# Optimization experiments

Hardware: AMD Instinct MI355X
Metric: run time of the kernel (lower is better)

## Reference

```python
import jax, jax.numpy as jnp
import numpy as np

B, T_CHAR, E, N_CHARS, T_TAG = 128, 256, 512, 128, 32


def _rn(k, shape, scale=1.0):
    return jax.random.normal(k, shape, dtype=jnp.float32) * scale


def setup_inputs() -> dict:
    key = jax.random.key(0)
    ks = jax.random.split(key, 24)
    W = 0.05  # param init scale
    tgt_idx = jax.random.randint(ks[4], (B, T_CHAR), 0, N_CHARS)
    return {
        "char_encoding": _rn(ks[0], (B, T_CHAR, E)),
        "char_hn": _rn(ks[1], (2, B, E // 2)),
        "char_cn": _rn(ks[2], (2, B, E // 2)),
        "tag_encoding": _rn(ks[3], (B, T_TAG, E)),
        "true_output_seq": jax.nn.one_hot(tgt_idx, N_CHARS, dtype=jnp.float32),
        # LSTMCell(n_chars -> E), torch gate order i,f,g,o
        "lstm_Wih": _rn(ks[5], (4 * E, N_CHARS), W),
        "lstm_Whh": _rn(ks[6], (4 * E, E), W),
        "lstm_bih": jnp.zeros((4 * E,), jnp.float32),
        "lstm_bhh": jnp.zeros((4 * E,), jnp.float32),
        # char MultiheadAttention (1 head)
        "ca_Wq": _rn(ks[7], (E, E), W), "ca_Wk": _rn(ks[8], (E, E), W), "ca_Wv": _rn(ks[9], (E, E), W),
        "ca_bq": jnp.zeros((E,), jnp.float32), "ca_bk": jnp.zeros((E,), jnp.float32), "ca_bv": jnp.zeros((E,), jnp.float32),
        "ca_Wo": _rn(ks[10], (E, E), W), "ca_bo": jnp.zeros((E,), jnp.float32),
        # tag MultiheadAttention (1 head)
        "ta_Wq": _rn(ks[11], (E, E), W), "ta_Wk": _rn(ks[12], (E, E), W), "ta_Wv": _rn(ks[13], (E, E), W),
        "ta_bq": jnp.zeros((E,), jnp.float32), "ta_bk": jnp.zeros((E,), jnp.float32), "ta_bv": jnp.zeros((E,), jnp.float32),
        "ta_Wo": _rn(ks[14], (E, E), W), "ta_bo": jnp.zeros((E,), jnp.float32),
        # output Linear(2E -> n_chars)
        "out_W": _rn(ks[15], (N_CHARS, 2 * E), W),
        "out_b": jnp.zeros((N_CHARS,), jnp.float32),
    }


def _attend(h, enc_K, enc_V, Wq, bq, Wo, bo):
    # single-head torch MHA: scale query by 1/sqrt(embed_dim)
    q = (h @ Wq.T + bq) * (1.0 / np.sqrt(E))          # [B,E]
    scores = jnp.einsum('be,bse->bs', q, enc_K)        # [B,S]
    a = jax.nn.softmax(scores, axis=-1)
    ctx = jnp.einsum('bs,bse->be', a, enc_V)           # [B,E]
    return ctx @ Wo.T + bo


def reference(char_encoding, char_hn, char_cn, tag_encoding, true_output_seq,
              lstm_Wih, lstm_Whh, lstm_bih, lstm_bhh,
              ca_Wq, ca_Wk, ca_Wv, ca_bq, ca_bk, ca_bv, ca_Wo, ca_bo,
              ta_Wq, ta_Wk, ta_Wv, ta_bq, ta_bk, ta_bv, ta_Wo, ta_bo,
              out_W, out_b):
    # K/V projections are step-invariant: hoist out of the decode loop
    Kc = char_encoding @ ca_Wk.T + ca_bk               # [B,Tc,E]
    Vc = char_encoding @ ca_Wv.T + ca_bv
    Kt = tag_encoding @ ta_Wk.T + ta_bk                # [B,Tt,E]
    Vt = tag_encoding @ ta_Wv.T + ta_bv

    h0 = jnp.concatenate([char_hn[0], char_hn[1]], axis=-1)  # [B,E]
    c0 = jnp.concatenate([char_cn[0], char_cn[1]], axis=-1)

    # teacher forcing: step 0 input is zeros, step t uses true_output_seq[:, t, :]
    x0 = jnp.zeros((char_encoding.shape[0], true_output_seq.shape[-1]), char_encoding.dtype)
    xs = jnp.concatenate([x0[:, None, :], true_output_seq[:, 1:, :]], axis=1)
    xs = jnp.swapaxes(xs, 0, 1)                        # [T,B,n_chars]

    def step(carry, x_t):
        h, c = carry
        gates = x_t @ lstm_Wih.T + lstm_bih + h @ lstm_Whh.T + lstm_bhh
        i, f, g, o = jnp.split(gates, 4, axis=-1)
        c1 = jax.nn.sigmoid(f) * c + jax.nn.sigmoid(i) * jnp.tanh(g)
        h1 = jax.nn.sigmoid(o) * jnp.tanh(c1)
        char_ctx = _attend(h1, Kc, Vc, ca_Wq, ca_bq, ca_Wo, ca_bo)
        tag_ctx = _attend(h1, Kt, Vt, ta_Wq, ta_bq, ta_Wo, ta_bo)
        agg = jax.nn.relu(jnp.concatenate([char_ctx, tag_ctx], axis=-1))  # [B,2E]
        out = agg @ out_W.T + out_b                    # [B,n_chars]
        return (h1, c1), out

    _, outs = jax.lax.scan(step, (h0, c0), xs)         # outs: [T,B,n_chars]
    return jnp.swapaxes(outs, 0, 1)                    # [B,T,n_chars]
```

## Files before the change

### kernel.cpp

```cpp
#include <hip/hip_runtime.h>
#include <cstdint>

#define BB 128
#define TT 256
#define EE 512
#define NC 128
#define STAG 32

#define NWG 64
#define SB 4
#define SC 16
#define NKV 2304

using bf = unsigned short;
typedef __attribute__((ext_vector_type(8))) short short8;
typedef __attribute__((ext_vector_type(8))) unsigned short ushort8;
typedef __attribute__((ext_vector_type(16))) float f32x16;
typedef unsigned long long u64;

static __device__ __forceinline__ float bf_lo(uint32_t u) { return __uint_as_float(u << 16); }
static __device__ __forceinline__ float bf_hi(uint32_t u) { return __uint_as_float(u & 0xFFFF0000u); }
static __device__ __forceinline__ float bfu(bf x) { return __uint_as_float(((uint32_t)x) << 16); }
static __device__ __forceinline__ uint32_t f2bf(float f) {
    uint32_t u = __float_as_uint(f);
    return (u + 0x7FFFu + ((u >> 16) & 1u)) >> 16;
}
static __device__ __forceinline__ float sigmoidf_(float x) { return 1.f / (1.f + expf(-x)); }

static __device__ __forceinline__ void bf8exp(const uint4 u, float* f) {
    f[0] = bf_lo(u.x); f[1] = bf_hi(u.x); f[2] = bf_lo(u.y); f[3] = bf_hi(u.y);
    f[4] = bf_lo(u.z); f[5] = bf_hi(u.z); f[6] = bf_lo(u.w); f[7] = bf_hi(u.w);
}

static __device__ __forceinline__ uint4 pack8bf(float4 a, float4 b) {
    uint4 o;
    o.x = (f2bf(a.y) << 16) | f2bf(a.x);
    o.y = (f2bf(a.w) << 16) | f2bf(a.z);
    o.z = (f2bf(b.y) << 16) | f2bf(b.x);
    o.w = (f2bf(b.w) << 16) | f2bf(b.z);
    return o;
}

static __device__ __forceinline__ uint32_t relu2bf(uint32_t x) {
    uint32_t lo = x & 0xFFFFu, hi = x >> 16;
    lo = (lo & 0x8000u) ? 0u : lo;
    hi = (hi & 0x8000u) ? 0u : hi;
    return lo | (hi << 16);
}

__global__ void diag_ws(float* __restrict__ out, float v, int n) {
    int i = blockIdx.x * 256 + threadIdx.x;
    if (i < n) out[i] = v;
}

__global__ void conv_f2b(const float* __restrict__ s, bf* __restrict__ d, int n) {
    int i = (blockIdx.x * 256 + threadIdx.x) * 4;
    if (i >= n) return;
    float4 v = *(const float4*)(s + i);
    ushort4 o = { (bf)f2bf(v.x), (bf)f2bf(v.y), (bf)f2bf(v.z), (bf)f2bf(v.w) };
    *(ushort4*)(d + i) = o;
}

struct W8 { const float* p[8]; };
__global__ void conv_w8(W8 ws, bf* __restrict__ d) {
    int m = blockIdx.y;
    int i = (blockIdx.x * 256 + threadIdx.x) * 4;
    float4 v = *(const float4*)(ws.p[m] + i);
    ushort4 o = { (bf)f2bf(v.x), (bf)f2bf(v.y), (bf)f2bf(v.z), (bf)f2bf(v.w) };
    *(ushort4*)(d + (size_t)m * 262144 + i) = o;
}

__global__ void h0_pack(const float* __restrict__ hn, bf* __restrict__ Hext) {
    int id = blockIdx.x * 256 + threadIdx.x;
    int b = id >> 9, e = id & 511;
    float v = (e < 256) ? hn[(size_t)b * 256 + e] : hn[(size_t)(BB + b) * 256 + (e - 256)];
    Hext[((size_t)(e >> 3) * BB + b) * 8 + (e & 7)] = (bf)f2bf(v);
}

__global__ void bt_prep2(const float* __restrict__ Whh, bf* __restrict__ Btg2) {
    int id = blockIdx.x * 256 + threadIdx.x;
    int row = id >> 6, chunk = (id & 63) * 8;
    int cg = row >> 7, n = row & 127;
    int r = (n & 3) * 512 + cg * 32 + (n >> 2);
    const float* src = Whh + (size_t)r * 512 + chunk;
    ushort8 o;
#pragma unroll
    for (int i = 0; i < 8; ++i) o[i] = (bf)f2bf(src[i]);
    *(ushort8*)(Btg2 + (size_t)row * 512 + chunk) = o;
}

__global__ void x_prep(const float* __restrict__ tos, int* __restrict__ xidx,
                       float* __restrict__ xval) {
    int id = blockIdx.x * 256 + threadIdx.x;
    int t = id >> 7, b = id & 127;
    int idx = 0; float val = 0.f;
    if (t > 0) {
        const float* row = tos + ((size_t)b * TT + t) * NC;
        for (int k = 0; k < NC; ++k) {
            float v = row[k];
            if (v != 0.f) { idx = k; val = v; }
        }
    }
    xidx[(size_t)t * BB + b] = idx;
    xval[(size_t)t * BB + b] = val;
}

static __device__ __forceinline__ int lds_off(int row, int colbyte) {
    return row * 128 + (colbyte ^ ((row & 7) << 4));
}

static __device__ __forceinline__ void worker_gemm(
    const float* __restrict__ Af, const bf* __restrict__ Wb,
    const float* __restrict__ bias, bf* __restrict__ C,
    int bm, int bn, char* smem)
{
    bf* As = (bf*)smem;
    bf* Bs = (bf*)(smem + 16384);
    const int tid = threadIdx.x;
    const int w = tid >> 6, l = tid & 63;
    const int wr = (w >> 1) * 64, wc = (w & 1) * 64;

    f32x16 acc[2][2];
#pragma unroll
    for (int i = 0; i < 2; ++i)
#pragma unroll
        for (int j = 0; j < 2; ++j)
#pragma unroll
            for (int r = 0; r < 16; ++r) acc[i][j][r] = 0.f;

    const int srow = tid >> 3;
    const int scolb = (tid & 7) * 16;
    const int scole = (tid & 7) * 8;

    for (int k0 = 0; k0 < 512; k0 += 64) {
#pragma unroll
        for (int pass = 0; pass < 4; ++pass) {
            int row = pass * 32 + srow;
            const float* ap = Af + (size_t)(bm + row) * 512 + k0 + scole;
            float4 v0 = *(const float4*)ap;
            float4 v1 = *(const float4*)(ap + 4);
            *(uint4*)(smem + lds_off(row, scolb)) = pack8bf(v0, v1);
            uint4 vb = *(const uint4*)(Wb + (size_t)(bn + row) * 512 + k0 + scole);
            *(uint4*)((char*)Bs + lds_off(row, scolb)) = vb;
        }
        __syncthreads();
#pragma unroll
        for (int kt = 0; kt < 4; ++kt) {
            const int cb = kt * 32 + (l >> 5) * 16;
            short8 af[2], bfr[2];
#pragma unroll
            for (int i = 0; i < 2; ++i) {
                af[i]  = *(const short8*)((char*)As + lds_off(wr + i * 32 + (l & 31), cb));
                bfr[i] = *(const short8*)((char*)Bs + lds_off(wc + i * 32 + (l & 31), cb));
            }
#pragma unroll
            for (int i = 0; i < 2; ++i)
#pragma unroll
                for (int j = 0; j < 2; ++j)
                    acc[i][j] = __builtin_amdgcn_mfma_f32_32x32x16_bf16(af[i], bfr[j], acc[i][j], 0, 0, 0);
        }
        __syncthreads();
    }

#pragma unroll
    for (int i = 0; i < 2; ++i)
#pragma unroll
        for (int j = 0; j < 2; ++j) {
            int n = bn + wc + j * 32 + (l & 31);
            float bv = bias[n];
#pragma unroll
            for (int r = 0; r < 16; ++r) {
                int m = bm + wr + i * 32 + (r & 3) + 8 * (r >> 2) + 4 * (l >> 5);
                C[(size_t)m * 512 + n] = (bf)f2bf(acc[i][j][r] + bv);
            }
        }
}

struct KVArgs {
    const float *Ac, *At;
    const bf *WcK, *WcV, *WtK, *WtV;
    const float *bcK, *bcV, *btK, *btV;
    bf *Kc, *Vc, *Kt, *Vt;
};

__global__ __launch_bounds__(256, 1) void lstm_fused(
    bf* __restrict__ Hext,
    const bf* __restrict__ Btg2,
    const float* __restrict__ Wih,
    const float* __restrict__ bih, const float* __restrict__ bhh,
    const float* __restrict__ cn,
    const int* __restrict__ xidx, const float* __restrict__ xval,
    char* __restrict__ flags,
    KVArgs kv)
{
    __shared__ __align__(16) char smem[66048];

    const int gb = blockIdx.x, tid = threadIdx.x;

    if (gb >= NWG) {
        int w = gb - NWG;
        if (w < 2048) {
            int v = w >> 10, t = w & 1023;
            worker_gemm(kv.Ac, v ? kv.WcV : kv.WcK, v ? kv.bcV : kv.bcK,
                        v ? kv.Vc : kv.Kc, (t >> 2) * 128, (t & 3) * 128, smem);
        } else {
            int w2 = w - 2048;
            int v = w2 >> 7, t = w2 & 127;
            worker_gemm(kv.At, v ? kv.WtV : kv.WtK, v ? kv.btV : kv.btK,
                        v ? kv.Vt : kv.Kt, (t >> 2) * 128, (t & 3) * 128, smem);
        }
        return;
    }

    bf*    Alds   = (bf*)smem;
    float* gatesf = (float*)smem;
    bf*    wihtp  = (bf*)(smem + 32768);
    float* biass  = (float*)(smem + 65536);

    const int g = gb;
    const int bh = g >> 4, cg = g & 15;

    for (int x = tid; x < 128 * NC; x += 256) {
        int n = x >> 7, k = x & 127;
        int r = (n & 3) * 512 + cg * 32 + (n >> 2);
        wihtp[k * 128 + n] = (bf)f2bf(Wih[(size_t)r * NC + k]);
    }
    if (tid < 128) {
        int r = (tid & 3) * 512 + cg * 32 + (tid >> 2);
        biass[tid] = bih[r] + bhh[r];
    }

    const int b_loc = tid >> 3, u = tid & 7;
    const int b_glob = bh * 32 + b_loc;
    float creg[4];
    {
        int j0 = cg * 32 + u * 4;
        const float* csrc = (cg < 8) ? (cn + (size_t)b_glob * 256 + j0)
                                     : (cn + (size_t)(BB + b_glob) * 256 + (j0 - 256));
#pragma unroll
        for (int i = 0; i < 4; ++i) creg[i] = csrc[i];
    }

    const int wv = tid >> 6, l = tid & 63;

    short8 breg[32];
    {
        const bf* bsrc = Btg2 + ((size_t)(cg * 128 + wv * 32 + (l & 31)) * 512)
                       + (l >> 5) * 8;
#pragma unroll
        for (int kt = 0; kt < 32; ++kt) breg[kt] = *(const short8*)(bsrc + kt * 16);
    }
    __syncthreads();

    const int sb = tid & 31, sg0 = tid >> 5;
    const int dst_lane = sb | ((sg0 & 1) << 5);
    bf* dstbase = Alds + (size_t)(sg0 >> 1) * 512 + dst_lane * 8;

    u64* Hw = (u64*)Hext;
    const size_t SLABB = (size_t)BB * EE * 2;
    const size_t SLAB64 = (size_t)BB * EE / 4;
    const size_t hst_off = (size_t)(cg * 4 + (u >> 1)) * 256 + b_glob * 2 + (u & 1);
    const bf* ards = Alds + l * 8;

    for (int t = 0; t < TT; ++t) {
        const char* At = (const char*)Hext + (size_t)t * SLABB
                       + (size_t)sg0 * 2048 + (size_t)(bh * 32 + sb) * 16;
        uint4 areg[8];
#pragma unroll
        for (int i = 0; i < 8; ++i) {
            asm volatile("global_load_dwordx4 %0, %1, off sc0 sc1"
                         : "=v"(areg[i]) : "v"(At + (size_t)i * 16384));
        }
        float xv = xval[(size_t)t * BB + b_glob];
        int   xi = xidx[(size_t)t * BB + b_glob];
        asm volatile("s_waitcnt vmcnt(0)" ::: "memory");
        __builtin_amdgcn_sched_barrier(0);
#pragma unroll
        for (int i = 0; i < 8; ++i)
            *(uint4*)(dstbase + (size_t)i * 2048) = areg[i];
        __syncthreads();

        f32x16 acc0, acc1;
#pragma unroll
        for (int i = 0; i < 16; ++i) { acc0[i] = 0.f; acc1[i] = 0.f; }
#pragma unroll
        for (int kt = 0; kt < 32; kt += 2) {
            short8 a0 = *(const short8*)(ards + (size_t)kt * 512);
            short8 a1 = *(const short8*)(ards + (size_t)(kt + 1) * 512);
            acc0 = __builtin_amdgcn_mfma_f32_32x32x16_bf16(a0, breg[kt], acc0, 0, 0, 0);
            acc1 = __builtin_amdgcn_mfma_f32_32x32x16_bf16(a1, breg[kt + 1], acc1, 0, 0, 0);
        }
        __syncthreads();
#pragma unroll
        for (int r = 0; r < 16; ++r) {
            int m = (r & 3) + 8 * (r >> 2) + 4 * (l >> 5);
            gatesf[m * 132 + wv * 32 + (l & 31)] = acc0[r] + acc1[r];
        }
        __syncthreads();

        {
            union { ushort4 v; u64 uu; } hout;
#pragma unroll
            for (int i = 0; i < 4; ++i) {
                int nb = (u * 4 + i) * 4;
                float4 ga  = *(const float4*)&gatesf[b_loc * 132 + nb];
                float4 bb4 = *(const float4*)&biass[nb];
                ushort4 xw = *(const ushort4*)&wihtp[xi * 128 + nb];
                float a0 = ga.x + bb4.x + xv * bfu(xw.x);
                float a1 = ga.y + bb4.y + xv * bfu(xw.y);
                float a2 = ga.z + bb4.z + xv * bfu(xw.z);
                float a3 = ga.w + bb4.w + xv * bfu(xw.w);
                float ig = sigmoidf_(a0);
                float fg = sigmoidf_(a1);
                float gg = tanhf(a2);
                float og = sigmoidf_(a3);
                creg[i] = fg * creg[i] + ig * gg;
                float hnew = og * tanhf(creg[i]);
                hout.v[i] = (bf)f2bf(hnew);
            }
            __hip_atomic_store(Hw + (size_t)(t + 1) * SLAB64 + hst_off, hout.uu,
                               __ATOMIC_RELAXED, __HIP_MEMORY_SCOPE_AGENT);
        }

        if (t + 1 < TT) {
            asm volatile("s_waitcnt vmcnt(0)" ::: "memory");
            __syncthreads();
            char* fb = flags + (size_t)(t + 1) * (SB * 2048) + (size_t)bh * 2048;
            if (tid == 0)
                __hip_atomic_store((int*)(fb + (size_t)cg * 128), 1,
                                   __ATOMIC_RELAXED, __HIP_MEMORY_SCOPE_SYSTEM);
            if (tid < 64) {
                const int* fp = (const int*)(fb + (size_t)(tid & 15) * 128);
                while (true) {
                    int v = __hip_atomic_load(fp, __ATOMIC_RELAXED,
                                              __HIP_MEMORY_SCOPE_SYSTEM);
                    if (__all(v != 0)) break;
                    __builtin_amdgcn_s_sleep(1);
                }
            }
            asm volatile("" ::: "memory");
            __syncthreads();
        }
    }
}

template <bool AH2>
__global__ __launch_bounds__(256) void gemm_mfma(
    const bf* __restrict__ A, const bf* __restrict__ Wb,
    const float* __restrict__ bias, bf* __restrict__ C,
    int M, float alpha)
{
    __shared__ __align__(16) bf As[128 * 64];
    __shared__ __align__(16) bf Bs[128 * 64];
    const int tid = threadIdx.x;
    const int bm = blockIdx.y * 128, bn = blockIdx.x * 128;
    const int w = tid >> 6, l = tid & 63;
    const int wr = (w >> 1) * 64, wc = (w & 1) * 64;

    f32x16 acc[2][2];
#pragma unroll
    for (int i = 0; i < 2; ++i)
#pragma unroll
        for (int j = 0; j < 2; ++j)
#pragma unroll
            for (int r = 0; r < 16; ++r) acc[i][j][r] = 0.f;

    const int srow = tid >> 3;
    const int scolb = (tid & 7) * 16;
    const int scole = (tid & 7) * 8;

    for (int k0 = 0; k0 < 512; k0 += 64) {
#pragma unroll
        for (int pass = 0; pass < 4; ++pass) {
            int row = pass * 32 + srow;
            const bf* ap;
            if constexpr (AH2) {
                int m = bm + row; int tt = m >> 7, bb_ = m & 127;
                int grp = (k0 + scole) >> 3;
                ap = A + ((((size_t)tt * 64 + grp) * BB + bb_) << 3);
            } else {
                ap = A + (size_t)(bm + row) * 512 + k0 + scole;
            }
            uint4 va = *(const uint4*)ap;
            *(uint4*)((char*)As + lds_off(row, scolb)) = va;
            uint4 vb = *(const uint4*)(Wb + (size_t)(bn + row) * 512 + k0 + scole);
            *(uint4*)((char*)Bs + lds_off(row, scolb)) = vb;
        }
        __syncthreads();
#pragma unroll
        for (int kt = 0; kt < 4; ++kt) {
            const int cb = kt * 32 + (l >> 5) * 16;
            short8 af[2], bfr[2];
#pragma unroll
            for (int i = 0; i < 2; ++i) {
                af[i]  = *(const short8*)((char*)As + lds_off(wr + i * 32 + (l & 31), cb));
                bfr[i] = *(const short8*)((char*)Bs + lds_off(wc + i * 32 + (l & 31), cb));
            }
#pragma unroll
            for (int i = 0; i < 2; ++i)
#pragma unroll
                for (int j = 0; j < 2; ++j)
                    acc[i][j] = __builtin_amdgcn_mfma_f32_32x32x16_bf16(af[i], bfr[j], acc[i][j], 0, 0, 0);
        }
        __syncthreads();
    }

#pragma unroll
    for (int i = 0; i < 2; ++i)
#pragma unroll
        for (int j = 0; j < 2; ++j) {
            int n = bn + wc + j * 32 + (l & 31);
            float bv = bias ? bias[n] : 0.f;
#pragma unroll
            for (int r = 0; r < 16; ++r) {
                int m = bm + wr + i * 32 + (r & 3) + 8 * (r >> 2) + 4 * (l >> 5);
                C[(size_t)m * 512 + n] = (bf)f2bf((acc[i][j][r] + bv) * alpha);
            }
        }
}

__global__ __launch_bounds__(256) void gemm_out(
    const bf* __restrict__ A1, const bf* __restrict__ A2,
    const bf* __restrict__ Wo,
    const float* __restrict__ bias, float* __restrict__ out)
{
    __shared__ __align__(16) bf As[128 * 64];
    __shared__ __align__(16) bf Bs[128 * 64];
    const int tid = threadIdx.x;
    const int bm = blockIdx.x * 128;
    const int w = tid >> 6, l = tid & 63;
    const int wr = (w >> 1) * 64, wc = (w & 1) * 64;

    f32x16 acc[2][2];
#pragma unroll
    for (int i = 0; i < 2; ++i)
#pragma unroll
        for (int j = 0; j < 2; ++j)
#pragma unroll
            for (int r = 0; r < 16; ++r) acc[i][j][r] = 0.f;

    const int srow = tid >> 3;
    const int scolb = (tid & 7) * 16;
    const int scole = (tid & 7) * 8;

    for (int k0 = 0; k0 < 1024; k0 += 64) {
        const bf* Asrc = (k0 < 512) ? A1 : A2;
        const int kk = k0 & 511;
#pragma unroll
        for (int pass = 0; pass < 4; ++pass) {
            int row = pass * 32 + srow;
            uint4 va = *(const uint4*)(Asrc + (size_t)(bm + row) * 512 + kk + scole);
            va.x = relu2bf(va.x); va.y = relu2bf(va.y);
            va.z = relu2bf(va.z); va.w = relu2bf(va.w);
            *(uint4*)((char*)As + lds_off(row, scolb)) = va;
            uint4 vb = *(const uint4*)(Wo + (size_t)row * 1024 + k0 + scole);
            *(uint4*)((char*)Bs + lds_off(row, scolb)) = vb;
        }
        __syncthreads();
#pragma unroll
        for (int kt = 0; kt < 4; ++kt) {
            const int cb = kt * 32 + (l >> 5) * 16;
            short8 af[2], bfr[2];
#pragma unroll
            for (int i = 0; i < 2; ++i) {
                af[i]  = *(const short8*)((char*)As + lds_off(wr + i * 32 + (l & 31), cb));
                bfr[i] = *(const short8*)((char*)Bs + lds_off(wc + i * 32 + (l & 31), cb));
            }
#pragma unroll
            for (int i = 0; i < 2; ++i)
#pragma unroll
                for (int j = 0; j < 2; ++j)
                    acc[i][j] = __builtin_amdgcn_mfma_f32_32x32x16_bf16(af[i], bfr[j], acc[i][j], 0, 0, 0);
        }
        __syncthreads();
    }

#pragma unroll
    for (int i = 0; i < 2; ++i)
#pragma unroll
        for (int j = 0; j < 2; ++j) {
            int n = wc + j * 32 + (l & 31);
            float bv = bias[n];
#pragma unroll
            for (int r = 0; r < 16; ++r) {
                int m = bm + wr + i * 32 + (r & 3) + 8 * (r >> 2) + 4 * (l >> 5);
                int tt = m >> 7, bb_ = m & 127;
                out[((size_t)bb_ * TT + tt) * NC + n] = acc[i][j][r] + bv;
            }
        }
}

template <int S>
__global__ __launch_bounds__(256) void attn_kernel(
    const bf* __restrict__ Q, const bf* __restrict__ Km,
    const bf* __restrict__ Vm, bf* __restrict__ ctx)
{
    constexpr int RT = 16;
    int t0 = blockIdx.x * RT;
    int b = blockIdx.y;
    int tid = threadIdx.x;

    __shared__ __align__(16) float qs[RT][EE];
    __shared__ float ps[RT][S];
    __shared__ float red[RT][17];
    __shared__ float rowsum[RT];

#pragma unroll
    for (int i = 0; i < RT * EE / (256 * 8); ++i) {
        int x = (i * 256 + tid) * 8;
        int r = x / EE, e = x % EE;
        uint4 u = *(const uint4*)&Q[((size_t)(t0 + r) * BB + b) * EE + e];
        float f[8]; bf8exp(u, f);
#pragma unroll
        for (int q = 0; q < 8; ++q) qs[r][e + q] = f[q];
    }
    __syncthreads();

    if constexpr (S >= 256) {
        int s = tid;
        float acc[RT] = {};
        const uint4* kp = (const uint4*)&Km[((size_t)b * S + s) * EE];
        for (int e8 = 0; e8 < EE / 8; ++e8) {
            float kf[8]; bf8exp(kp[e8], kf);
#pragma unroll
            for (int r = 0; r < RT; ++r) {
                float a = 0.f;
#pragma unroll
                for (int q = 0; q < 8; ++q) a += qs[r][e8 * 8 + q] * kf[q];
                acc[r] += a;
            }
        }
#pragma unroll
        for (int r = 0; r < RT; ++r) ps[r][s] = acc[r];
    } else {
        constexpr int KS = 256 / S;
        constexpr int EC = EE / KS;
        __shared__ float pp[KS][RT][S];
        int s = tid & (S - 1);
        int kq = tid / S;
        float acc[RT] = {};
        const uint4* kp = (const uint4*)&Km[((size_t)b * S + s) * EE + kq * EC];
        for (int e8 = 0; e8 < EC / 8; ++e8) {
            float kf[8]; bf8exp(kp[e8], kf);
#pragma unroll
            for (int r = 0; r < RT; ++r) {
                float a = 0.f;
#pragma unroll
                for (int q = 0; q < 8; ++q) a += qs[r][kq * EC + e8 * 8 + q] * kf[q];
                acc[r] += a;
            }
        }
#pragma unroll
        for (int r = 0; r < RT; ++r) pp[kq][r][s] = acc[r];
        __syncthreads();
        for (int x = tid; x < RT * S; x += 256) {
            int r = x / S, ss = x % S;
            float v = 0.f;
#pragma unroll
            for (int q = 0; q < KS; ++q) v += pp[q][r][ss];
            ps[r][ss] = v;
        }
    }
    __syncthreads();

    {
        int r = tid >> 4, l = tid & 15;
        float m = -1e30f;
        for (int s = l; s < S; s += 16) m = fmaxf(m, ps[r][s]);
        red[r][l] = m;
        __syncthreads();
        for (int w = 8; w >= 1; w >>= 1) {
            if (l < w) red[r][l] = fmaxf(red[r][l], red[r][l + w]);
            __syncthreads();
        }
        float mm = red[r][0];
        float sum = 0.f;
        for (int s = l; s < S; s += 16) {
            float e = expf(ps[r][s] - mm);
            ps[r][s] = e;
            sum += e;
        }
        __syncthreads();
        red[r][l] = sum;
        __syncthreads();
        for (int w = 8; w >= 1; w >>= 1) {
            if (l < w) red[r][l] += red[r][l + w];
            __syncthreads();
        }
        if (l == 0) rowsum[r] = red[r][0];
    }
    __syncthreads();

    {
        float acc0[RT] = {}, acc1[RT] = {};
        for (int s = 0; s < S; ++s) {
            float v0 = bfu(Vm[((size_t)b * S + s) * EE + tid]);
            float v1 = bfu(Vm[((size_t)b * S + s) * EE + tid + 256]);
#pragma unroll
            for (int r = 0; r < RT; ++r) {
                float p = ps[r][s];
                acc0[r] += p * v0;
                acc1[r] += p * v1;
            }
        }
#pragma unroll
        for (int r = 0; r < RT; ++r) {
            float inv = 1.f / rowsum[r];
            size_t row = (size_t)(t0 + r) * BB + b;
            ctx[row * EE + tid] = (bf)f2bf(acc0[r] * inv);
            ctx[row * EE + tid + 256] = (bf)f2bf(acc1[r] * inv);
        }
    }
}

extern "C" void kernel_launch(void* const* d_in, const int* in_sizes, int n_in,
                              void* d_out, int out_size, void* d_ws, size_t ws_size,
                              hipStream_t stream) {
    const float* char_enc = (const float*)d_in[0];
    const float* char_hn  = (const float*)d_in[1];
    const float* char_cn  = (const float*)d_in[2];
    const float* tag_enc  = (const float*)d_in[3];
    const float* tos      = (const float*)d_in[4];
    const float* Wih = (const float*)d_in[5];
    const float* Whh = (const float*)d_in[6];
    const float* bih = (const float*)d_in[7];
    const float* bhh = (const float*)d_in[8];
    const float* caWq = (const float*)d_in[9],  *caWk = (const float*)d_in[10], *caWv = (const float*)d_in[11];
    const float* cabq = (const float*)d_in[12], *cabk = (const float*)d_in[13], *cabv = (const float*)d_in[14];
    const float* caWo = (const float*)d_in[15], *cabo = (const float*)d_in[16];
    const float* taWq = (const float*)d_in[17], *taWk = (const float*)d_in[18], *taWv = (const float*)d_in[19];
    const float* tabq = (const float*)d_in[20], *tabk = (const float*)d_in[21], *tabv = (const float*)d_in[22];
    const float* taWo = (const float*)d_in[23], *tabo = (const float*)d_in[24];
    const float* outW = (const float*)d_in[25], *outb = (const float*)d_in[26];
    float* out = (float*)d_out;

    const size_t SZ  = (size_t)TT * BB * EE;
    const size_t SZT = (size_t)BB * STAG * EE;
    const size_t SLAB = (size_t)BB * EE;
    const size_t HEXT = SZ + SLAB;
    const size_t FLAGB = (size_t)TT * SB * 2048;

    const size_t NEED = FLAGB + HEXT * 2 + 4 * SZ * 2 + 2 * SZT * 2
                      + (size_t)SC * 128 * EE * 2 + (size_t)TT * BB * 8
                      + (8 * 262144 + 131072) * 2;
    if (ws_size < NEED) {
        diag_ws<<<dim3((out_size + 255) / 256), dim3(256), 0, stream>>>(
            out, (float)((double)ws_size / 1048576.0), out_size);
        return;
    }

    char* w = (char*)d_ws;
    char* flags = w;             w += FLAGB;
    bf* Hext = (bf*)w;           w += HEXT * 2;
    bf* Kc = (bf*)w;             w += SZ * 2;
    bf* Vc = (bf*)w;             w += SZ * 2;
    bf* Qc = (bf*)w;             w += SZ * 2;
    bf* Qt = (bf*)w;             w += SZ * 2;
    bf* Kt = (bf*)w;             w += SZT * 2;
    bf* Vt = (bf*)w;             w += SZT * 2;
    bf* Btg2 = (bf*)w;           w += (size_t)SC * 128 * EE * 2;
    int* xidx = (int*)w;         w += (size_t)TT * BB * 4;
    float* xval = (float*)w;     w += (size_t)TT * BB * 4;
    bf* Wbf = (bf*)w;            w += 8 * 262144 * 2;
    bf* WoutB = (bf*)w;          w += 131072 * 2;

    const bf* Hh = Hext + SLAB;
    const float QSCALE = 0.044194173824159216f;
    const int M = TT * BB;

    bf* WbcaK = Wbf + 0 * 262144; bf* WbcaV = Wbf + 1 * 262144;
    bf* WbcaQ = Wbf + 2 * 262144; bf* WbcaO = Wbf + 3 * 262144;
    bf* WbtaK = Wbf + 4 * 262144; bf* WbtaV = Wbf + 5 * 262144;
    bf* WbtaQ = Wbf + 6 * 262144; bf* WbtaO = Wbf + 7 * 262144;

    hipMemsetAsync(flags, 0, FLAGB, stream);
    h0_pack<<<dim3(256), dim3(256), 0, stream>>>(char_hn, Hext);
    bt_prep2<<<dim3(512), dim3(256), 0, stream>>>(Whh, Btg2);
    x_prep<<<dim3(128), dim3(256), 0, stream>>>(tos, xidx, xval);
    W8 w8; w8.p[0] = caWk; w8.p[1] = caWv; w8.p[2] = caWq; w8.p[3] = caWo;
    w8.p[4] = taWk; w8.p[5] = taWv; w8.p[6] = taWq; w8.p[7] = taWo;
    conv_w8<<<dim3(256, 8), dim3(256), 0, stream>>>(w8, Wbf);
    conv_f2b<<<dim3(128), dim3(256), 0, stream>>>(outW, WoutB, 131072);

    KVArgs kv;
    kv.Ac = char_enc; kv.At = tag_enc;
    kv.WcK = WbcaK; kv.WcV = WbcaV; kv.WtK = WbtaK; kv.WtV = WbtaV;
    kv.bcK = cabk; kv.bcV = cabv; kv.btK = tabk; kv.btV = tabv;
    kv.Kc = Kc; kv.Vc = Vc; kv.Kt = Kt; kv.Vt = Vt;
    lstm_fused<<<dim3(NWG + NKV), dim3(256), 0, stream>>>(
        Hext, Btg2, Wih, bih, bhh, char_cn, xidx, xval, flags, kv);

    gemm_mfma<true><<<dim3(4, 256), dim3(256), 0, stream>>>(Hh, WbcaQ, cabq, Qc, M, QSCALE);
    gemm_mfma<true><<<dim3(4, 256), dim3(256), 0, stream>>>(Hh, WbtaQ, tabq, Qt, M, QSCALE);

    attn_kernel<256><<<dim3(TT / 16, BB), dim3(256), 0, stream>>>(Qc, Kc, Vc, Qc);
    attn_kernel<32><<<dim3(TT / 16, BB), dim3(256), 0, stream>>>(Qt, Kt, Vt, Qt);

    gemm_mfma<false><<<dim3(4, 256), dim3(256), 0, stream>>>(Qc, WbcaO, cabo, Kc, M, 1.f);
    gemm_mfma<false><<<dim3(4, 256), dim3(256), 0, stream>>>(Qt, WbtaO, tabo, Vc, M, 1.f);

    gemm_out<<<dim3(256), dim3(256), 0, stream>>>(Kc, Vc, WoutB, outb, out);
}
```

Baseline: 1.716 ms.

## Fuse Q projection, attention, and output projection into one MFMA kernel per attention

Replaces the separate Q-projection GEMMs, scalar-FMA attention kernels and output-projection GEMMs with a single attn_fused kernel per attention that computes Q, the scores, the softmax, P·V and the Wo projection on MFMA, keeping intermediates in LDS. The K/V worker GEMMs now write V transposed (per batch, feature-major) so the P·V MFMA can read contiguous operands. This removes the global round trips for Q and the context plus the fp32 scalar attention math. In exchange, each block rereads Wq, Wo and K/V straight from global memory without LDS staging, and the grid is smaller (8x128 blocks at one block per CU), which may limit occupancy.

```diff
diff --git a/kernel.cpp b/kernel.cpp
--- a/kernel.cpp
+++ b/kernel.cpp
@@ -18,19 +18,12 @@
 typedef __attribute__((ext_vector_type(16))) float f32x16;
 typedef unsigned long long u64;
 
-static __device__ __forceinline__ float bf_lo(uint32_t u) { return __uint_as_float(u << 16); }
-static __device__ __forceinline__ float bf_hi(uint32_t u) { return __uint_as_float(u & 0xFFFF0000u); }
 static __device__ __forceinline__ float bfu(bf x) { return __uint_as_float(((uint32_t)x) << 16); }
 static __device__ __forceinline__ uint32_t f2bf(float f) {
     uint32_t u = __float_as_uint(f);
     return (u + 0x7FFFu + ((u >> 16) & 1u)) >> 16;
 }
 static __device__ __forceinline__ float sigmoidf_(float x) { return 1.f / (1.f + expf(-x)); }
-
-static __device__ __forceinline__ void bf8exp(const uint4 u, float* f) {
-    f[0] = bf_lo(u.x); f[1] = bf_hi(u.x); f[2] = bf_lo(u.y); f[3] = bf_hi(u.y);
-    f[4] = bf_lo(u.z); f[5] = bf_hi(u.z); f[6] = bf_lo(u.w); f[7] = bf_hi(u.w);
-}
 
 static __device__ __forceinline__ uint4 pack8bf(float4 a, float4 b) {
     uint4 o;
@@ -109,6 +102,7 @@
     return row * 128 + (colbyte ^ ((row & 7) << 4));
 }
 
+template <int MODE>
 static __device__ __forceinline__ void worker_gemm(
     const float* __restrict__ Af, const bf* __restrict__ Wb,
     const float* __restrict__ bias, bf* __restrict__ C,
@@ -139,7 +133,7 @@
             const float* ap = Af + (size_t)(bm + row) * 512 + k0 + scole;
             float4 v0 = *(const float4*)ap;
             float4 v1 = *(const float4*)(ap + 4);
-            *(uint4*)(smem + lds_off(row, scolb)) = pack8bf(v0, v1);
+            *(uint4*)((char*)As + lds_off(row, scolb)) = pack8bf(v0, v1);
             uint4 vb = *(const uint4*)(Wb + (size_t)(bn + row) * 512 + k0 + scole);
             *(uint4*)((char*)Bs + lds_off(row, scolb)) = vb;
         }
@@ -171,7 +165,16 @@
 #pragma unroll
             for (int r = 0; r < 16; ++r) {
                 int m = bm + wr + i * 32 + (r & 3) + 8 * (r >> 2) + 4 * (l >> 5);
-                C[(size_t)m * 512 + n] = (bf)f2bf(acc[i][j][r] + bv);
+                bf v = (bf)f2bf(acc[i][j][r] + bv);
+                if constexpr (MODE == 0) {
+                    C[(size_t)m * 512 + n] = v;
+                } else if constexpr (MODE == 1) {
+                    int b = m >> 8, s = m & 255;
+                    C[((size_t)b * 512 + n) * 256 + s] = v;
+                } else {
+                    int b = m >> 5, s = m & 31;
+                    C[((size_t)b * 512 + n) * 32 + s] = v;
+                }
             }
         }
 }
@@ -180,7 +183,7 @@
     const float *Ac, *At;
     const bf *WcK, *WcV, *WtK, *WtV;
     const float *bcK, *bcV, *btK, *btV;
-    bf *Kc, *Vc, *Kt, *Vt;
+    bf *Kc, *VcT, *Kt, *VtT;
 };
 
 __global__ __launch_bounds__(256, 1) void lstm_fused(
@@ -199,15 +202,17 @@
 
     if (gb >= NWG) {
         int w = gb - NWG;
-        if (w < 2048) {
-            int v = w >> 10, t = w & 1023;
-            worker_gemm(kv.Ac, v ? kv.WcV : kv.WcK, v ? kv.bcV : kv.bcK,
-                        v ? kv.Vc : kv.Kc, (t >> 2) * 128, (t & 3) * 128, smem);
+        if (w < 1024) {
+            worker_gemm<0>(kv.Ac, kv.WcK, kv.bcK, kv.Kc, (w >> 2) * 128, (w & 3) * 128, smem);
+        } else if (w < 2048) {
+            int t = w - 1024;
+            worker_gemm<1>(kv.Ac, kv.WcV, kv.bcV, kv.VcT, (t >> 2) * 128, (t & 3) * 128, smem);
+        } else if (w < 2176) {
+            int t = w - 2048;
+            worker_gemm<0>(kv.At, kv.WtK, kv.btK, kv.Kt, (t >> 2) * 128, (t & 3) * 128, smem);
         } else {
-            int w2 = w - 2048;
-            int v = w2 >> 7, t = w2 & 127;
-            worker_gemm(kv.At, v ? kv.WtV : kv.WtK, v ? kv.btV : kv.btK,
-                        v ? kv.Vt : kv.Kt, (t >> 2) * 128, (t & 3) * 128, smem);
+            int t = w - 2176;
+            worker_gemm<2>(kv.At, kv.WtV, kv.btV, kv.VtT, (t >> 2) * 128, (t & 3) * 128, smem);
         }
         return;
     }
@@ -344,79 +349,159 @@
     }
 }
 
-template <bool AH2>
-__global__ __launch_bounds__(256) void gemm_mfma(
-    const bf* __restrict__ A, const bf* __restrict__ Wb,
-    const float* __restrict__ bias, bf* __restrict__ C,
-    int M, float alpha)
+template <int S>
+__global__ __launch_bounds__(256, 1) void attn_fused(
+    const bf* __restrict__ Hext,
+    const bf* __restrict__ Wq, const float* __restrict__ bq,
+    const bf* __restrict__ Km,
+    const bf* __restrict__ VT,
+    const bf* __restrict__ Wo, const float* __restrict__ bo,
+    bf* __restrict__ occ)
 {
-    __shared__ __align__(16) bf As[128 * 64];
-    __shared__ __align__(16) bf Bs[128 * 64];
-    const int tid = threadIdx.x;
-    const int bm = blockIdx.y * 128, bn = blockIdx.x * 128;
-    const int w = tid >> 6, l = tid & 63;
-    const int wr = (w >> 1) * 64, wc = (w & 1) * 64;
-
-    f32x16 acc[2][2];
-#pragma unroll
-    for (int i = 0; i < 2; ++i)
-#pragma unroll
-        for (int j = 0; j < 2; ++j)
-#pragma unroll
-            for (int r = 0; r < 16; ++r) acc[i][j][r] = 0.f;
-
-    const int srow = tid >> 3;
-    const int scolb = (tid & 7) * 16;
-    const int scole = (tid & 7) * 8;
-
-    for (int k0 = 0; k0 < 512; k0 += 64) {
-#pragma unroll
-        for (int pass = 0; pass < 4; ++pass) {
-            int row = pass * 32 + srow;
-            const bf* ap;
-            if constexpr (AH2) {
-                int m = bm + row; int tt = m >> 7, bb_ = m & 127;
-                int grp = (k0 + scole) >> 3;
-                ap = A + ((((size_t)tt * 64 + grp) * BB + bb_) << 3);
-            } else {
-                ap = A + (size_t)(bm + row) * 512 + k0 + scole;
-            }
-            uint4 va = *(const uint4*)ap;
-            *(uint4*)((char*)As + lds_off(row, scolb)) = va;
-            uint4 vb = *(const uint4*)(Wb + (size_t)(bn + row) * 512 + k0 + scole);
-            *(uint4*)((char*)Bs + lds_off(row, scolb)) = vb;
-        }
-        __syncthreads();
-#pragma unroll
-        for (int kt = 0; kt < 4; ++kt) {
-            const int cb = kt * 32 + (l >> 5) * 16;
-            short8 af[2], bfr[2];
-#pragma unroll
-            for (int i = 0; i < 2; ++i) {
-                af[i]  = *(const short8*)((char*)As + lds_off(wr + i * 32 + (l & 31), cb));
-                bfr[i] = *(const short8*)((char*)Bs + lds_off(wc + i * 32 + (l & 31), cb));
-            }
-#pragma unroll
-            for (int i = 0; i < 2; ++i)
-#pragma unroll
-                for (int j = 0; j < 2; ++j)
-                    acc[i][j] = __builtin_amdgcn_mfma_f32_32x32x16_bf16(af[i], bfr[j], acc[i][j], 0, 0, 0);
-        }
-        __syncthreads();
-    }
-
-#pragma unroll
-    for (int i = 0; i < 2; ++i)
-#pragma unroll
-        for (int j = 0; j < 2; ++j) {
-            int n = bn + wc + j * 32 + (l & 31);
-            float bv = bias ? bias[n] : 0.f;
+    constexpr int SP = S + 8;
+    __shared__ __align__(16) bf    Qs[32][520];
+    __shared__ __align__(16) float scs[32][SP];
+    __shared__ __align__(16) bf    Ps[32][SP];
+
+    const float QSCALE = 0.044194173824159216f;
+    const int t0 = blockIdx.x * 32, b = blockIdx.y;
+    const int tid = threadIdx.x, wv = tid >> 6, l = tid & 63;
+    const int lm = l & 31, lh = l >> 5;
+
+    {
+        f32x16 qa[4];
+#pragma unroll
+        for (int nt = 0; nt < 4; ++nt)
+#pragma unroll
+            for (int r = 0; r < 16; ++r) qa[nt][r] = 0.f;
+#pragma unroll 4
+        for (int kt = 0; kt < 32; ++kt) {
+            short8 a = *(const short8*)(Hext
+                + (((size_t)(t0 + lm + 1) * 64 + kt * 2 + lh) * 1024 + (size_t)b * 8));
+#pragma unroll
+            for (int nt = 0; nt < 4; ++nt) {
+                int n = wv * 128 + nt * 32 + lm;
+                short8 w = *(const short8*)(Wq + (size_t)n * 512 + kt * 16 + lh * 8);
+                qa[nt] = __builtin_amdgcn_mfma_f32_32x32x16_bf16(a, w, qa[nt], 0, 0, 0);
+            }
+        }
+#pragma unroll
+        for (int nt = 0; nt < 4; ++nt) {
+            int n = wv * 128 + nt * 32 + lm;
+            float bv = bq[n];
 #pragma unroll
             for (int r = 0; r < 16; ++r) {
-                int m = bm + wr + i * 32 + (r & 3) + 8 * (r >> 2) + 4 * (l >> 5);
-                C[(size_t)m * 512 + n] = (bf)f2bf((acc[i][j][r] + bv) * alpha);
-            }
-        }
+                int m = (r & 3) + 8 * (r >> 2) + 4 * lh;
+                Qs[m][n] = (bf)f2bf((qa[nt][r] + bv) * QSCALE);
+            }
+        }
+    }
+    __syncthreads();
+
+    {
+        constexpr int NJ = (S == 256) ? 2 : 1;
+        f32x16 sa[NJ];
+#pragma unroll
+        for (int j = 0; j < NJ; ++j)
+#pragma unroll
+            for (int r = 0; r < 16; ++r) sa[j][r] = 0.f;
+#pragma unroll 4
+        for (int kt = 0; kt < 32; ++kt) {
+            short8 a = *(const short8*)&Qs[lm][kt * 16 + lh * 8];
+#pragma unroll
+            for (int j = 0; j < NJ; ++j) {
+                int s = ((S == 256) ? (wv * 64 + j * 32) : 0) + lm;
+                short8 k8 = *(const short8*)(Km + ((size_t)b * S + s) * 512 + kt * 16 + lh * 8);
+                sa[j] = __builtin_amdgcn_mfma_f32_32x32x16_bf16(a, k8, sa[j], 0, 0, 0);
+            }
+        }
+#pragma unroll
+        for (int j = 0; j < NJ; ++j) {
+            int s = ((S == 256) ? (wv * 64 + j * 32) : 0) + lm;
+#pragma unroll
+            for (int r = 0; r < 16; ++r) {
+                int m = (r & 3) + 8 * (r >> 2) + 4 * lh;
+                scs[m][s] = sa[j][r];
+            }
+        }
+    }
+    __syncthreads();
+
+    {
+        int r = tid >> 3, lg = tid & 7;
+        float mx = -1e30f;
+        for (int c = lg; c < S; c += 8) mx = fmaxf(mx, scs[r][c]);
+#pragma unroll
+        for (int d = 1; d < 8; d <<= 1) mx = fmaxf(mx, __shfl_xor(mx, d));
+        float sum = 0.f;
+        for (int c = lg; c < S; c += 8) {
+            float e = expf(scs[r][c] - mx);
+            scs[r][c] = e;
+            sum += e;
+        }
+#pragma unroll
+        for (int d = 1; d < 8; d <<= 1) sum += __shfl_xor(sum, d);
+        float inv = 1.f / sum;
+        for (int c = lg; c < S; c += 8) Ps[r][c] = (bf)f2bf(scs[r][c] * inv);
+    }
+    __syncthreads();
+
+    {
+        f32x16 ca[4];
+#pragma unroll
+        for (int nt = 0; nt < 4; ++nt)
+#pragma unroll
+            for (int r = 0; r < 16; ++r) ca[nt][r] = 0.f;
+#pragma unroll
+        for (int kt = 0; kt < S / 16; ++kt) {
+            short8 a = *(const short8*)&Ps[lm][kt * 16 + lh * 8];
+#pragma unroll
+            for (int nt = 0; nt < 4; ++nt) {
+                int n = wv * 128 + nt * 32 + lm;
+                short8 v8 = *(const short8*)(VT + ((size_t)b * 512 + n) * S + kt * 16 + lh * 8);
+                ca[nt] = __builtin_amdgcn_mfma_f32_32x32x16_bf16(a, v8, ca[nt], 0, 0, 0);
+            }
+        }
+        __syncthreads();
+#pragma unroll
+        for (int nt = 0; nt < 4; ++nt) {
+            int n = wv * 128 + nt * 32 + lm;
+#pragma unroll
+            for (int r = 0; r < 16; ++r) {
+                int m = (r & 3) + 8 * (r >> 2) + 4 * lh;
+                Qs[m][n] = (bf)f2bf(ca[nt][r]);
+            }
+        }
+    }
+    __syncthreads();
+
+    {
+        f32x16 oa[4];
+#pragma unroll
+        for (int nt = 0; nt < 4; ++nt)
+#pragma unroll
+            for (int r = 0; r < 16; ++r) oa[nt][r] = 0.f;
+#pragma unroll 4
+        for (int kt = 0; kt < 32; ++kt) {
+            short8 a = *(const short8*)&Qs[lm][kt * 16 + lh * 8];
+#pragma unroll
+            for (int nt = 0; nt < 4; ++nt) {
+                int n = wv * 128 + nt * 32 + lm;
+                short8 w = *(const short8*)(Wo + (size_t)n * 512 + kt * 16 + lh * 8);
+                oa[nt] = __builtin_amdgcn_mfma_f32_32x32x16_bf16(a, w, oa[nt], 0, 0, 0);
+            }
+        }
+#pragma unroll
+        for (int nt = 0; nt < 4; ++nt) {
+            int n = wv * 128 + nt * 32 + lm;
+            float bv = bo[n];
+#pragma unroll
+            for (int r = 0; r < 16; ++r) {
+                int m = (r & 3) + 8 * (r >> 2) + 4 * lh;
+                occ[((size_t)(t0 + m) * BB + b) * 512 + n] = (bf)f2bf(oa[nt][r] + bv);
+            }
+        }
+    }
 }
 
 __global__ __launch_bounds__(256) void gemm_out(
@@ -488,129 +573,6 @@
                 out[((size_t)bb_ * TT + tt) * NC + n] = acc[i][j][r] + bv;
             }
         }
-}
-
-template <int S>
-__global__ __launch_bounds__(256) void attn_kernel(
-    const bf* __restrict__ Q, const bf* __restrict__ Km,
-    const bf* __restrict__ Vm, bf* __restrict__ ctx)
-{
-    constexpr int RT = 16;
-    int t0 = blockIdx.x * RT;
-    int b = blockIdx.y;
-    int tid = threadIdx.x;
-
-    __shared__ __align__(16) float qs[RT][EE];
-    __shared__ float ps[RT][S];
-    __shared__ float red[RT][17];
-    __shared__ float rowsum[RT];
-
-#pragma unroll
-    for (int i = 0; i < RT * EE / (256 * 8); ++i) {
-        int x = (i * 256 + tid) * 8;
-        int r = x / EE, e = x % EE;
-        uint4 u = *(const uint4*)&Q[((size_t)(t0 + r) * BB + b) * EE + e];
-        float f[8]; bf8exp(u, f);
-#pragma unroll
-        for (int q = 0; q < 8; ++q) qs[r][e + q] = f[q];
-    }
-    __syncthreads();
-
-    if constexpr (S >= 256) {
-        int s = tid;
-        float acc[RT] = {};
-        const uint4* kp = (const uint4*)&Km[((size_t)b * S + s) * EE];
-        for (int e8 = 0; e8 < EE / 8; ++e8) {
-            float kf[8]; bf8exp(kp[e8], kf);
-#pragma unroll
-            for (int r = 0; r < RT; ++r) {
-                float a = 0.f;
-#pragma unroll
-                for (int q = 0; q < 8; ++q) a += qs[r][e8 * 8 + q] * kf[q];
-                acc[r] += a;
-            }
-        }
-#pragma unroll
-        for (int r = 0; r < RT; ++r) ps[r][s] = acc[r];
-    } else {
-        constexpr int KS = 256 / S;
-        constexpr int EC = EE / KS;
-        __shared__ float pp[KS][RT][S];
-        int s = tid & (S - 1);
-        int kq = tid / S;
-        float acc[RT] = {};
-        const uint4* kp = (const uint4*)&Km[((size_t)b * S + s) * EE + kq * EC];
-        for (int e8 = 0; e8 < EC / 8; ++e8) {
-            float kf[8]; bf8exp(kp[e8], kf);
-#pragma unroll
-            for (int r = 0; r < RT; ++r) {
-                float a = 0.f;
-#pragma unroll
-                for (int q = 0; q < 8; ++q) a += qs[r][kq * EC + e8 * 8 + q] * kf[q];
-                acc[r] += a;
-            }
-        }
-#pragma unroll
-        for (int r = 0; r < RT; ++r) pp[kq][r][s] = acc[r];
-        __syncthreads();
-        for (int x = tid; x < RT * S; x += 256) {
-            int r = x / S, ss = x % S;
-            float v = 0.f;
-#pragma unroll
-            for (int q = 0; q < KS; ++q) v += pp[q][r][ss];
-            ps[r][ss] = v;
-        }
-    }
-    __syncthreads();
-
-    {
-        int r = tid >> 4, l = tid & 15;
-        float m = -1e30f;
-        for (int s = l; s < S; s += 16) m = fmaxf(m, ps[r][s]);
-        red[r][l] = m;
-        __syncthreads();
-        for (int w = 8; w >= 1; w >>= 1) {
-            if (l < w) red[r][l] = fmaxf(red[r][l], red[r][l + w]);
-            __syncthreads();
-        }
-        float mm = red[r][0];
-        float sum = 0.f;
-        for (int s = l; s < S; s += 16) {
-            float e = expf(ps[r][s] - mm);
-            ps[r][s] = e;
-            sum += e;
-        }
-        __syncthreads();
-        red[r][l] = sum;
-        __syncthreads();
-        for (int w = 8; w >= 1; w >>= 1) {
-            if (l < w) red[r][l] += red[r][l + w];
-            __syncthreads();
-        }
-        if (l == 0) rowsum[r] = red[r][0];
-    }
-    __syncthreads();
-
-    {
-        float acc0[RT] = {}, acc1[RT] = {};
-        for (int s = 0; s < S; ++s) {
-            float v0 = bfu(Vm[((size_t)b * S + s) * EE + tid]);
-            float v1 = bfu(Vm[((size_t)b * S + s) * EE + tid + 256]);
-#pragma unroll
-            for (int r = 0; r < RT; ++r) {
-                float p = ps[r][s];
-                acc0[r] += p * v0;
-                acc1[r] += p * v1;
-            }
-        }
-#pragma unroll
-        for (int r = 0; r < RT; ++r) {
-            float inv = 1.f / rowsum[r];
-            size_t row = (size_t)(t0 + r) * BB + b;
-            ctx[row * EE + tid] = (bf)f2bf(acc0[r] * inv);
-            ctx[row * EE + tid + 256] = (bf)f2bf(acc1[r] * inv);
-        }
-    }
 }
 
 extern "C" void kernel_launch(void* const* d_in, const int* in_sizes, int n_in,
@@ -653,20 +615,16 @@
     char* flags = w;             w += FLAGB;
     bf* Hext = (bf*)w;           w += HEXT * 2;
     bf* Kc = (bf*)w;             w += SZ * 2;
-    bf* Vc = (bf*)w;             w += SZ * 2;
-    bf* Qc = (bf*)w;             w += SZ * 2;
-    bf* Qt = (bf*)w;             w += SZ * 2;
+    bf* VcT = (bf*)w;            w += SZ * 2;
+    bf* Occ = (bf*)w;            w += SZ * 2;
+    bf* Oct = (bf*)w;            w += SZ * 2;
     bf* Kt = (bf*)w;             w += SZT * 2;
-    bf* Vt = (bf*)w;             w += SZT * 2;
+    bf* VtT = (bf*)w;            w += SZT * 2;
     bf* Btg2 = (bf*)w;           w += (size_t)SC * 128 * EE * 2;
     int* xidx = (int*)w;         w += (size_t)TT * BB * 4;
     float* xval = (float*)w;     w += (size_t)TT * BB * 4;
     bf* Wbf = (bf*)w;            w += 8 * 262144 * 2;
     bf* WoutB = (bf*)w;          w += 131072 * 2;
-
-    const bf* Hh = Hext + SLAB;
-    const float QSCALE = 0.044194173824159216f;
-    const int M = TT * BB;
 
     bf* WbcaK = Wbf + 0 * 262144; bf* WbcaV = Wbf + 1 * 262144;
     bf* WbcaQ = Wbf + 2 * 262144; bf* WbcaO = Wbf + 3 * 262144;
@@ -686,18 +644,14 @@
     kv.Ac = char_enc; kv.At = tag_enc;
     kv.WcK = WbcaK; kv.WcV = WbcaV; kv.WtK = WbtaK; kv.WtV = WbtaV;
     kv.bcK = cabk; kv.bcV = cabv; kv.btK = tabk; kv.btV = tabv;
-    kv.Kc = Kc; kv.Vc = Vc; kv.Kt = Kt; kv.Vt = Vt;
+    kv.Kc = Kc; kv.VcT = VcT; kv.Kt = Kt; kv.VtT = VtT;
     lstm_fused<<<dim3(NWG + NKV), dim3(256), 0, stream>>>(
         Hext, Btg2, Wih, bih, bhh, char_cn, xidx, xval, flags, kv);
 
-    gemm_mfma<true><<<dim3(4, 256), dim3(256), 0, stream>>>(Hh, WbcaQ, cabq, Qc, M, QSCALE);
-    gemm_mfma<true><<<dim3(4, 256), dim3(256), 0, stream>>>(Hh, WbtaQ, tabq, Qt, M, QSCALE);
-
-    attn_kernel<256><<<dim3(TT / 16, BB), dim3(256), 0, stream>>>(Qc, Kc, Vc, Qc);
-    attn_kernel<32><<<dim3(TT / 16, BB), dim3(256), 0, stream>>>(Qt, Kt, Vt, Qt);
-
-    gemm_mfma<false><<<dim3(4, 256), dim3(256), 0, stream>>>(Qc, WbcaO, cabo, Kc, M, 1.f);
-    gemm_mfma<false><<<dim3(4, 256), dim3(256), 0, stream>>>(Qt, WbtaO, tabo, Vc, M, 1.f);
-
-    gemm_out<<<dim3(256), dim3(256), 0, stream>>>(Kc, Vc, WoutB, outb, out);
-}
+    attn_fused<256><<<dim3(TT / 32, BB), dim3(256), 0, stream>>>(
+        Hext, WbcaQ, cabq, Kc, VcT, WbcaO, cabo, Occ);
+    attn_fused<32><<<dim3(TT / 32, BB), dim3(256), 0, stream>>>(
+        Hext, WbtaQ, tabq, Kt, VtT, WbtaO, tabo, Oct);
+
+    gemm_out<<<dim3(256), dim3(256), 0, stream>>>(Occ, Oct, WoutB, outb, out);
+}
```

Result: faster. 1.561 ms (-9.0%).
